# Kernel optimization log

Hardware: AMD Instinct MI355X
Metric: run time of the kernel (lower is better)

## Reference

```python
import jax, jax.numpy as jnp
import numpy as np

N = 10000        # total_node
IN_SIZE = 128
OUT_SIZE = 128


def setup_inputs() -> dict:
    key = jax.random.key(0)
    k_adj, k_x, k_wn, k_ws = jax.random.split(key, 4)
    adj = jax.random.uniform(k_adj, (N, N), dtype=jnp.float32)           # package[1]
    old_node_embedding = jax.random.normal(k_x, (N, IN_SIZE), dtype=jnp.float32)
    # nn.Linear weights are stored [out, in]
    W_nei = jax.random.normal(k_wn, (OUT_SIZE, IN_SIZE), dtype=jnp.float32) * (1.0 / np.sqrt(IN_SIZE))
    W_self = jax.random.normal(k_ws, (OUT_SIZE, IN_SIZE), dtype=jnp.float32) * (1.0 / np.sqrt(IN_SIZE))
    return {
        "adj": adj,
        "old_node_embedding": old_node_embedding,
        "W_nei": W_nei,
        "W_self": W_self,
        "out_size": OUT_SIZE,
        "use_divce": 0,
    }


def reference(adj, old_node_embedding, W_nei, W_self, out_size, use_divce):
    # Vectorized form of the per-node torch loop:
    #   nei_gather[n]   = adj[n, :] @ X                (torch.mm per node)
    #   nei_info[n]     = nei_gather[n] @ W_nei^T      (nei_update1)
    #   self_info[n]    = X[n] @ W_self^T              (self_node_update1)
    #   new_emb[n]      = act(nei_info[n] + self_info[n])
    # active_method fixed to tanh.
    nei_gather = adj @ old_node_embedding                         # [N, in]
    nei_info = nei_gather @ W_nei.T                               # [N, out]
    self_info = old_node_embedding @ W_self.T                     # [N, out]
    return jnp.tanh(nei_info + self_info)
```

## Files before the change

### kernel.cpp

```cpp
#include <hip/hip_runtime.h>
#include <cmath>


#define N_NODES 10000
#define EMB 128
#define XNT_STRIDE 10240
#define KC 768
#define NKCH 14
#define LDSW 40

typedef __bf16 bf16x8 __attribute__((ext_vector_type(8)));
typedef float  f32x4  __attribute__((ext_vector_type(4)));

__device__ __forceinline__ bf16x8 bzero8() {
    bf16x8 v;
#pragma unroll
    for (int i = 0; i < 8; ++i) v[i] = (__bf16)0.0f;
    return v;
}

__global__ __launch_bounds__(256) void prep_kernel(
    const float* __restrict__ X, const float* __restrict__ Wn,
    __bf16* __restrict__ xnt_hi, __bf16* __restrict__ xnt_lo)
{
    __shared__ float Xl[32 * EMB];
    const int tid = threadIdx.x;
    const int n0 = blockIdx.x * 32;

#pragma unroll
    for (int i = 0; i < 4; ++i) {
        int idx = tid + i * 256;
        int r = idx >> 5;
        int c4 = (idx & 31) << 2;
        int row = n0 + r;
        float4 v = make_float4(0.f, 0.f, 0.f, 0.f);
        if (row < N_NODES) v = *(const float4*)(X + (size_t)row * EMB + c4);
        *(float4*)(Xl + r * EMB + c4) = v;
    }
    __syncthreads();

    const int c = tid & 127;
    const int half = tid >> 7;
    const float* wrow = Wn + c * EMB;

    float acc[16];
#pragma unroll
    for (int r = 0; r < 16; ++r) acc[r] = 0.f;

    for (int k4 = 0; k4 < 32; ++k4) {
        float4 w = *(const float4*)(wrow + k4 * 4);
#pragma unroll
        for (int r = 0; r < 16; ++r) {
            float4 x = *(const float4*)(Xl + (half * 16 + r) * EMB + k4 * 4);
            acc[r] += x.x * w.x + x.y * w.y + x.z * w.z + x.w * w.w;
        }
    }

    size_t base = (size_t)c * XNT_STRIDE + n0 + half * 16;
#pragma unroll
    for (int r = 0; r < 16; ++r) {
        int row = n0 + half * 16 + r;
        if (row < N_NODES) {
            float f = acc[r];
            __bf16 h = (__bf16)f;
            __bf16 l = (__bf16)(f - (float)h);
            xnt_hi[base + r] = h;
            xnt_lo[base + r] = l;
        }
    }
}

__device__ __forceinline__ void g_load(
    const float* __restrict__ arow_p, bool arv,
    const __bf16* __restrict__ bh_p, const __bf16* __restrict__ bl_p,
    int k0, int kc_end, int akq, int bkq, float4 av[4], bf16x8 bv[4])
{
    int ak = k0 + akq * 16;
#pragma unroll
    for (int i = 0; i < 4; ++i) {
        float4 v = make_float4(0.f, 0.f, 0.f, 0.f);
        int k = ak + i * 4;
        if (arv && k < kc_end) v = *(const float4*)(arow_p + k);
        av[i] = v;
    }
    int bk = k0 + bkq * 16;
    if (bk < kc_end) {
        bv[0] = *(const bf16x8*)(bh_p + bk);
        bv[1] = *(const bf16x8*)(bh_p + bk + 8);
        bv[2] = *(const bf16x8*)(bl_p + bk);
        bv[3] = *(const bf16x8*)(bl_p + bk + 8);
    } else {
        bv[0] = bv[1] = bv[2] = bv[3] = bzero8();
    }
}

__global__ __launch_bounds__(256, 2) void gemm_kernel(
    const float* __restrict__ adj, const __bf16* __restrict__ xnt_hi,
    const __bf16* __restrict__ xnt_lo, float* __restrict__ Y)
{
    __shared__ __bf16 Ah[128 * LDSW];
    __shared__ __bf16 Al[128 * LDSW];
    __shared__ __bf16 Bh[128 * LDSW];
    __shared__ __bf16 Bl[128 * LDSW];

    const int tid = threadIdx.x;
    const int m0 = blockIdx.x * 128;
    const int kc0 = blockIdx.y * KC;
    const int kc_end = min(kc0 + KC, N_NODES);
    const int nsub = (kc_end - kc0 + 31) >> 5;

    const int lane = tid & 63;
    const int wave = tid >> 6;
    const int wm = (wave & 1) * 64;
    const int wn = (wave >> 1) * 64;
    const int fr = lane & 15;
    const int q = lane >> 4;

    const int am = tid >> 1, akq = tid & 1;
    const bool arv = (m0 + am) < N_NODES;
    const float* arow_p = adj + (size_t)(m0 + am) * N_NODES;
    const int bc = tid >> 1, bkq = tid & 1;
    const __bf16* bh_p = xnt_hi + (size_t)bc * XNT_STRIDE;
    const __bf16* bl_p = xnt_lo + (size_t)bc * XNT_STRIDE;

    f32x4 acc[4][4];
#pragma unroll
    for (int mt = 0; mt < 4; ++mt)
#pragma unroll
        for (int nt = 0; nt < 4; ++nt)
#pragma unroll
            for (int e = 0; e < 4; ++e) acc[mt][nt][e] = 0.f;

    float4 av[4];
    bf16x8 bv[4];
    g_load(arow_p, arv, bh_p, bl_p, kc0, kc_end, akq, bkq, av, bv);

    for (int ks = 0; ks < nsub; ++ks) {
        bf16x8 ahv[2], alv[2];
#pragma unroll
        for (int i = 0; i < 16; ++i) {
            float f = ((const float*)av)[i];
            __bf16 h = (__bf16)f;
            __bf16 l = (__bf16)(f - (float)h);
            ahv[i >> 3][i & 7] = h;
            alv[i >> 3][i & 7] = l;
        }
        *(bf16x8*)&Ah[am * LDSW + akq * 16]     = ahv[0];
        *(bf16x8*)&Ah[am * LDSW + akq * 16 + 8] = ahv[1];
        *(bf16x8*)&Al[am * LDSW + akq * 16]     = alv[0];
        *(bf16x8*)&Al[am * LDSW + akq * 16 + 8] = alv[1];
        *(bf16x8*)&Bh[bc * LDSW + bkq * 16]     = bv[0];
        *(bf16x8*)&Bh[bc * LDSW + bkq * 16 + 8] = bv[1];
        *(bf16x8*)&Bl[bc * LDSW + bkq * 16]     = bv[2];
        *(bf16x8*)&Bl[bc * LDSW + bkq * 16 + 8] = bv[3];
        __syncthreads();

        float4 av2[4];
        bf16x8 bv2[4];
        g_load(arow_p, arv, bh_p, bl_p, kc0 + (ks + 1) * 32, kc_end, akq, bkq, av2, bv2);

        bf16x8 a_h[4], a_l[4], b_h[4], b_l[4];
#pragma unroll
        for (int t = 0; t < 4; ++t) {
            a_h[t] = *(const bf16x8*)&Ah[(wm + t * 16 + fr) * LDSW + q * 8];
            a_l[t] = *(const bf16x8*)&Al[(wm + t * 16 + fr) * LDSW + q * 8];
            b_h[t] = *(const bf16x8*)&Bh[(wn + t * 16 + fr) * LDSW + q * 8];
            b_l[t] = *(const bf16x8*)&Bl[(wn + t * 16 + fr) * LDSW + q * 8];
        }
#pragma unroll
        for (int mt = 0; mt < 4; ++mt)
#pragma unroll
            for (int nt = 0; nt < 4; ++nt) {
                acc[mt][nt] = __builtin_amdgcn_mfma_f32_16x16x32_bf16(a_h[mt], b_h[nt], acc[mt][nt], 0, 0, 0);
                acc[mt][nt] = __builtin_amdgcn_mfma_f32_16x16x32_bf16(a_h[mt], b_l[nt], acc[mt][nt], 0, 0, 0);
                acc[mt][nt] = __builtin_amdgcn_mfma_f32_16x16x32_bf16(a_l[mt], b_h[nt], acc[mt][nt], 0, 0, 0);
            }
        __syncthreads();
#pragma unroll
        for (int i = 0; i < 4; ++i) { av[i] = av2[i]; bv[i] = bv2[i]; }
    }

#pragma unroll
    for (int mt = 0; mt < 4; ++mt) {
        int rbase = m0 + wm + mt * 16 + q * 4;
#pragma unroll
        for (int nt = 0; nt < 4; ++nt) {
            int col = wn + nt * 16 + fr;
#pragma unroll
            for (int r = 0; r < 4; ++r) {
                int row = rbase + r;
                if (row < N_NODES)
                    atomicAdd(Y + (size_t)row * EMB + col, acc[mt][nt][r]);
            }
        }
    }
}

__global__ __launch_bounds__(256) void epi_kernel(
    const float* __restrict__ X, const float* __restrict__ Wself,
    float* __restrict__ out)
{
    __shared__ float Xl[32 * EMB];
    const int tid = threadIdx.x;
    const int n0 = blockIdx.x * 32;

#pragma unroll
    for (int i = 0; i < 4; ++i) {
        int idx = tid + i * 256;
        int r = idx >> 5;
        int c4 = (idx & 31) << 2;
        int row = n0 + r;
        float4 v = make_float4(0.f, 0.f, 0.f, 0.f);
        if (row < N_NODES) v = *(const float4*)(X + (size_t)row * EMB + c4);
        *(float4*)(Xl + r * EMB + c4) = v;
    }
    __syncthreads();

    const int c = tid & 127;
    const int half = tid >> 7;
    const float* wrow = Wself + c * EMB;

    float acc[16];
#pragma unroll
    for (int r = 0; r < 16; ++r) acc[r] = 0.f;

    for (int k4 = 0; k4 < 32; ++k4) {
        float4 w = *(const float4*)(wrow + k4 * 4);
#pragma unroll
        for (int r = 0; r < 16; ++r) {
            float4 x = *(const float4*)(Xl + (half * 16 + r) * EMB + k4 * 4);
            acc[r] += x.x * w.x + x.y * w.y + x.z * w.z + x.w * w.w;
        }
    }

#pragma unroll
    for (int r = 0; r < 16; ++r) {
        int row = n0 + half * 16 + r;
        if (row < N_NODES) {
            size_t i = (size_t)row * EMB + c;
            out[i] = tanhf(out[i] + acc[r]);
        }
    }
}

__global__ __launch_bounds__(256) void gemm0_kernel(
    const float* __restrict__ adj, const float* __restrict__ X,
    float* __restrict__ Y)
{
    __shared__ float As[128 * 33];
    __shared__ float Xs[32 * 132];
    const int tid = threadIdx.x;
    const int m0 = blockIdx.x * 128;
    const int kc0 = blockIdx.y * KC;
    const int kc_end = min(kc0 + KC, N_NODES);
    const int nsub = (kc_end - kc0 + 31) >> 5;

    const int am = tid >> 1, akq = tid & 1;
    const bool arv = (m0 + am) < N_NODES;
    const float* arow_p = adj + (size_t)(m0 + am) * N_NODES;
    const int xr = tid >> 3, xq = tid & 7;
    const int mq = tid >> 4, nq = tid & 15;

    float acc[8][8];
#pragma unroll
    for (int i = 0; i < 8; ++i)
#pragma unroll
        for (int j = 0; j < 8; ++j) acc[i][j] = 0.f;

    for (int ks = 0; ks < nsub; ++ks) {
        int k0 = kc0 + ks * 32;
#pragma unroll
        for (int i = 0; i < 4; ++i) {
            int k = k0 + akq * 16 + i * 4;
            float4 v = make_float4(0.f, 0.f, 0.f, 0.f);
            if (arv && k < kc_end) v = *(const float4*)(arow_p + k);
            float* d = As + am * 33 + akq * 16 + i * 4;
            d[0] = v.x; d[1] = v.y; d[2] = v.z; d[3] = v.w;
        }
#pragma unroll
        for (int i = 0; i < 4; ++i) {
            int c0 = xq * 16 + i * 4;
            int krow = k0 + xr;
            float4 v = make_float4(0.f, 0.f, 0.f, 0.f);
            if (krow < kc_end) v = *(const float4*)(X + (size_t)krow * EMB + c0);
            *(float4*)(Xs + xr * 132 + c0) = v;
        }
        __syncthreads();
        for (int k = 0; k < 32; ++k) {
            float a8[8];
#pragma unroll
            for (int i = 0; i < 8; ++i) a8[i] = As[(mq * 8 + i) * 33 + k];
            float4 x0 = *(const float4*)(Xs + k * 132 + nq * 8);
            float4 x1 = *(const float4*)(Xs + k * 132 + nq * 8 + 4);
            float x8[8] = { x0.x, x0.y, x0.z, x0.w, x1.x, x1.y, x1.z, x1.w };
#pragma unroll
            for (int i = 0; i < 8; ++i)
#pragma unroll
                for (int j = 0; j < 8; ++j) acc[i][j] += a8[i] * x8[j];
        }
        __syncthreads();
    }
#pragma unroll
    for (int i = 0; i < 8; ++i) {
        int row = m0 + mq * 8 + i;
        if (row < N_NODES) {
#pragma unroll
            for (int j = 0; j < 8; ++j)
                atomicAdd(Y + (size_t)row * EMB + nq * 8 + j, acc[i][j]);
        }
    }
}

__global__ __launch_bounds__(256) void epi0_kernel(
    const float* __restrict__ X, const float* __restrict__ Wn,
    const float* __restrict__ Ws, float* __restrict__ out)
{
    __shared__ float Xl[32 * EMB];
    __shared__ float Yl[32 * EMB];
    const int tid = threadIdx.x;
    const int n0 = blockIdx.x * 32;

#pragma unroll
    for (int i = 0; i < 4; ++i) {
        int idx = tid + i * 256;
        int r = idx >> 5;
        int c4 = (idx & 31) << 2;
        int row = n0 + r;
        float4 vx = make_float4(0.f, 0.f, 0.f, 0.f);
        float4 vy = vx;
        if (row < N_NODES) {
            vx = *(const float4*)(X + (size_t)row * EMB + c4);
            vy = *(const float4*)(out + (size_t)row * EMB + c4);
        }
        *(float4*)(Xl + r * EMB + c4) = vx;
        *(float4*)(Yl + r * EMB + c4) = vy;
    }
    __syncthreads();

    const int c = tid & 127;
    const int half = tid >> 7;
    const float* wn = Wn + c * EMB;
    const float* ws = Ws + c * EMB;

    float accn[16], accs[16];
#pragma unroll
    for (int r = 0; r < 16; ++r) { accn[r] = 0.f; accs[r] = 0.f; }

    for (int k4 = 0; k4 < 32; ++k4) {
        float4 a = *(const float4*)(wn + k4 * 4);
        float4 b = *(const float4*)(ws + k4 * 4);
#pragma unroll
        for (int r = 0; r < 16; ++r) {
            float4 y = *(const float4*)(Yl + (half * 16 + r) * EMB + k4 * 4);
            float4 x = *(const float4*)(Xl + (half * 16 + r) * EMB + k4 * 4);
            accn[r] += y.x * a.x + y.y * a.y + y.z * a.z + y.w * a.w;
            accs[r] += x.x * b.x + x.y * b.y + x.z * b.z + x.w * b.w;
        }
    }
#pragma unroll
    for (int r = 0; r < 16; ++r) {
        int row = n0 + half * 16 + r;
        if (row < N_NODES)
            out[(size_t)row * EMB + c] = tanhf(accn[r] + accs[r]);
    }
}

extern "C" void kernel_launch(void* const* d_in, const int* in_sizes, int n_in,
                              void* d_out, int out_size, void* d_ws, size_t ws_size,
                              hipStream_t stream) {
    const float* adj = (const float*)d_in[0];
    const float* X   = (const float*)d_in[1];
    const float* Wn  = (const float*)d_in[2];
    const float* Ws  = (const float*)d_in[3];
    float* out = (float*)d_out;

    const size_t xnt_elems = (size_t)EMB * XNT_STRIDE;
    const size_t need = xnt_elems * 2 * sizeof(unsigned short);

    hipMemsetAsync(d_out, 0, (size_t)N_NODES * EMB * sizeof(float), stream);

    if (ws_size >= need) {
        __bf16* xh = (__bf16*)d_ws;
        __bf16* xl = xh + xnt_elems;
        prep_kernel<<<(N_NODES + 31) / 32, 256, 0, stream>>>(X, Wn, xh, xl);
        gemm_kernel<<<dim3((N_NODES + 127) / 128, NKCH), 256, 0, stream>>>(adj, xh, xl, out);
        epi_kernel<<<(N_NODES + 31) / 32, 256, 0, stream>>>(X, Ws, out);
    } else {
        gemm0_kernel<<<dim3((N_NODES + 127) / 128, NKCH), 256, 0, stream>>>(adj, X, out);
        epi0_kernel<<<(N_NODES + 31) / 32, 256, 0, stream>>>(X, Wn, Ws, out);
    }
}
```

Before: 681.4 us.

## Replace split-K atomics with per-chunk partial buffers reduced in epilogue

The split-K GEMM now writes each K-chunk's partial result to its own workspace slice instead of using atomicAdd into the output, and the epilogue sums the 13 partials before applying tanh. This drops the output memset and the atomic traffic, but adds about 67 MB of partial writes and reads. The K chunk goes from 768 to 800 so there are 13 chunks instead of 14. The prep kernel now stores its bf16 hi/lo values as 8-wide vectors instead of scalar stores.

```diff
diff --git a/kernel.cpp b/kernel.cpp
--- a/kernel.cpp
+++ b/kernel.cpp
@@ -5,8 +5,8 @@
 #define N_NODES 10000
 #define EMB 128
 #define XNT_STRIDE 10240
-#define KC 768
-#define NKCH 14
+#define KC 800
+#define NKCH 13
 #define LDSW 40
 
 typedef __bf16 bf16x8 __attribute__((ext_vector_type(8)));
@@ -56,17 +56,21 @@
         }
     }
 
-    size_t base = (size_t)c * XNT_STRIDE + n0 + half * 16;
-#pragma unroll
-    for (int r = 0; r < 16; ++r) {
-        int row = n0 + half * 16 + r;
-        if (row < N_NODES) {
+    if (n0 + half * 16 < N_NODES) {
+        bf16x8 h0, h1, l0, l1;
+#pragma unroll
+        for (int r = 0; r < 16; ++r) {
             float f = acc[r];
             __bf16 h = (__bf16)f;
             __bf16 l = (__bf16)(f - (float)h);
-            xnt_hi[base + r] = h;
-            xnt_lo[base + r] = l;
-        }
+            if (r < 8) { h0[r] = h; l0[r] = l; }
+            else       { h1[r - 8] = h; l1[r - 8] = l; }
+        }
+        size_t base = (size_t)c * XNT_STRIDE + n0 + half * 16;
+        *(bf16x8*)(xnt_hi + base)     = h0;
+        *(bf16x8*)(xnt_hi + base + 8) = h1;
+        *(bf16x8*)(xnt_lo + base)     = l0;
+        *(bf16x8*)(xnt_lo + base + 8) = l1;
     }
 }
 
@@ -96,7 +100,7 @@
 
 __global__ __launch_bounds__(256, 2) void gemm_kernel(
     const float* __restrict__ adj, const __bf16* __restrict__ xnt_hi,
-    const __bf16* __restrict__ xnt_lo, float* __restrict__ Y)
+    const __bf16* __restrict__ xnt_lo, float* __restrict__ Ppart)
 {
     __shared__ __bf16 Ah[128 * LDSW];
     __shared__ __bf16 Al[128 * LDSW];
@@ -180,6 +184,7 @@
         for (int i = 0; i < 4; ++i) { av[i] = av2[i]; bv[i] = bv2[i]; }
     }
 
+    float* P = Ppart + (size_t)blockIdx.y * ((size_t)N_NODES * EMB);
 #pragma unroll
     for (int mt = 0; mt < 4; ++mt) {
         int rbase = m0 + wm + mt * 16 + q * 4;
@@ -190,7 +195,7 @@
             for (int r = 0; r < 4; ++r) {
                 int row = rbase + r;
                 if (row < N_NODES)
-                    atomicAdd(Y + (size_t)row * EMB + col, acc[mt][nt][r]);
+                    P[(size_t)row * EMB + col] = acc[mt][nt][r];
             }
         }
     }
@@ -198,7 +203,7 @@
 
 __global__ __launch_bounds__(256) void epi_kernel(
     const float* __restrict__ X, const float* __restrict__ Wself,
-    float* __restrict__ out)
+    const float* __restrict__ Ppart, float* __restrict__ out)
 {
     __shared__ float Xl[32 * EMB];
     const int tid = threadIdx.x;
@@ -233,13 +238,18 @@
         }
     }
 
-#pragma unroll
-    for (int r = 0; r < 16; ++r) {
-        int row = n0 + half * 16 + r;
-        if (row < N_NODES) {
-            size_t i = (size_t)row * EMB + c;
-            out[i] = tanhf(out[i] + acc[r]);
-        }
+    if (n0 + half * 16 < N_NODES) {
+        const size_t rb = (size_t)(n0 + half * 16) * EMB + c;
+#pragma unroll
+        for (int p = 0; p < NKCH; ++p) {
+            const float* Pp = Ppart + (size_t)p * ((size_t)N_NODES * EMB) + rb;
+#pragma unroll
+            for (int r = 0; r < 16; ++r)
+                acc[r] += Pp[(size_t)r * EMB];
+        }
+#pragma unroll
+        for (int r = 0; r < 16; ++r)
+            out[rb + (size_t)r * EMB] = tanhf(acc[r]);
     }
 }
 
@@ -375,17 +385,18 @@
     float* out = (float*)d_out;
 
     const size_t xnt_elems = (size_t)EMB * XNT_STRIDE;
-    const size_t need = xnt_elems * 2 * sizeof(unsigned short);
-
-    hipMemsetAsync(d_out, 0, (size_t)N_NODES * EMB * sizeof(float), stream);
-
-    if (ws_size >= need) {
+    const size_t xnt_bytes = xnt_elems * 2 * sizeof(unsigned short);
+    const size_t part_bytes = (size_t)NKCH * N_NODES * EMB * sizeof(float);
+
+    if (ws_size >= xnt_bytes + part_bytes) {
         __bf16* xh = (__bf16*)d_ws;
         __bf16* xl = xh + xnt_elems;
+        float* Ppart = (float*)((char*)d_ws + xnt_bytes);
         prep_kernel<<<(N_NODES + 31) / 32, 256, 0, stream>>>(X, Wn, xh, xl);
-        gemm_kernel<<<dim3((N_NODES + 127) / 128, NKCH), 256, 0, stream>>>(adj, xh, xl, out);
-        epi_kernel<<<(N_NODES + 31) / 32, 256, 0, stream>>>(X, Ws, out);
+        gemm_kernel<<<dim3((N_NODES + 127) / 128, NKCH), 256, 0, stream>>>(adj, xh, xl, Ppart);
+        epi_kernel<<<(N_NODES + 31) / 32, 256, 0, stream>>>(X, Ws, Ppart, out);
     } else {
+        hipMemsetAsync(d_out, 0, (size_t)N_NODES * EMB * sizeof(float), stream);
         gemm0_kernel<<<dim3((N_NODES + 127) / 128, NKCH), 256, 0, stream>>>(adj, X, out);
         epi0_kernel<<<(N_NODES + 31) / 32, 256, 0, stream>>>(X, Wn, Ws, out);
     }
```

Measured after the change: 636.5 us. 6.6% less time.
